# Kernel optimization log

Hardware: AMD Instinct MI355X
Metric: run time of the kernel (lower is better)

The kernel has to match this reference:

```python
import jax, jax.numpy as jnp
import numpy as np

BH = 32  # block_h
BW = 32  # block_w
M, K, N = 4096, 4096, 4096  # tokens, in_features, out_features


def setup_inputs() -> dict:
    key = jax.random.key(0)
    k1, k2, k3, k4 = jax.random.split(key, 4)
    data = jax.random.normal(k1, (M, K), dtype=jnp.float32)
    weight = jax.random.normal(k2, (N, K), dtype=jnp.float32) * 0.02
    bias = jax.random.normal(k3, (N,), dtype=jnp.float32) * 0.02
    # elementwise 0/1 mask over the weight matrix
    mask = jax.random.randint(k4, (N, K), 0, 2, dtype=jnp.int32)
    # conv bias of the 1x1-channel block-summing conv; chosen so ~half the
    # 32x32 blocks (sum ~ Binomial(1024, 0.5)) end up inactive
    conv_bias = jnp.full((1,), -512.0, dtype=jnp.float32)
    return {"data": data, "weight": weight, "bias": bias, "mask": mask,
            "conv_bias": conv_bias}


def reference(data, weight, bias, mask, conv_bias):
    n_out, n_in = weight.shape
    nH, nW = n_out // BH, n_in // BW
    # conv2d with all-ones (BH,BW) kernel, stride (BH,BW) == per-block sum + bias
    block_sum = mask.astype(jnp.float32).reshape(nH, BH, nW, BW).sum(axis=(1, 3))
    block_mask = (block_sum + conv_bias[0]) > 0  # [nH, nW] bool
    # dds matmul (trans_b=True): zero inactive weight blocks, out = data @ W^T
    w_blocks = weight.reshape(nH, BH, nW, BW)
    w_masked = (w_blocks * block_mask[:, None, :, None].astype(weight.dtype)
                ).reshape(n_out, n_in)
    out = jnp.einsum('mk,nk->mn', data, w_masked) + bias
    return out
```

## Files before the change

### kernel.cpp

```cpp
#include <hip/hip_runtime.h>
#include <hip/hip_bf16.h>
#include <stdint.h>

#define M_DIM 4096
#define N_DIM 4096
#define K_DIM 4096
#define NH 128
#define NW 128
#define NKT 64

typedef short bf16x8 __attribute__((ext_vector_type(8)));
typedef short bf16x4 __attribute__((ext_vector_type(4)));
typedef float f32x4 __attribute__((ext_vector_type(4)));

#define MFMA(a, b, c) __builtin_amdgcn_mfma_f32_16x16x32_bf16((a), (b), (c), 0, 0, 0)

__device__ __forceinline__ short f2bf(float f) {
  union { float f; unsigned u; } c; c.f = f;
  unsigned u = c.u;
  unsigned r = (u + 0x7fffu + ((u >> 16) & 1u)) >> 16;
  return (short)r;
}

__global__ __launch_bounds__(256) void k_block_mask(const int* __restrict__ mask,
                                                    const float* __restrict__ conv_bias,
                                                    int* __restrict__ bm) {
  const int bw = blockIdx.x, bh = blockIdx.y;
  const int t = threadIdx.x;
  const int row = t >> 3;
  const int c4 = (t & 7) << 2;
  const int4* p = (const int4*)(mask + (size_t)(bh * 32 + row) * K_DIM + bw * 32 + c4);
  int4 v = *p;
  int s = v.x + v.y + v.z + v.w;
#pragma unroll
  for (int off = 32; off > 0; off >>= 1) s += __shfl_down(s, off);
  __shared__ int red[4];
  if ((t & 63) == 0) red[t >> 6] = s;
  __syncthreads();
  if (t == 0) {
    float tot = (float)(red[0] + red[1] + red[2] + red[3]) + conv_bias[0];
    bm[bh * NW + bw] = (tot > 0.0f) ? 1 : 0;
  }
}

__global__ __launch_bounds__(256) void k_cvt_data(const float* __restrict__ in,
                                                  short* __restrict__ ob) {
  size_t i = (size_t)blockIdx.x * 256 + threadIdx.x;
  f32x4 v = ((const f32x4*)in)[i];
  bf16x4 o;
  o[0] = f2bf(v[0]); o[1] = f2bf(v[1]); o[2] = f2bf(v[2]); o[3] = f2bf(v[3]);
  ((bf16x4*)ob)[i] = o;
}

__global__ __launch_bounds__(256) void k_cvt_weight(const float* __restrict__ w,
                                                    const int* __restrict__ bm,
                                                    short* __restrict__ ob) {
  size_t i = (size_t)blockIdx.x * 256 + threadIdx.x;
  int n = (int)(i >> 10);
  int k = ((int)i & 1023) << 2;
  float m = bm[((n >> 5) << 7) + (k >> 5)] ? 1.0f : 0.0f;
  f32x4 v = ((const f32x4*)w)[i];
  bf16x4 o;
  o[0] = f2bf(v[0] * m); o[1] = f2bf(v[1] * m);
  o[2] = f2bf(v[2] * m); o[3] = f2bf(v[3] * m);
  ((bf16x4*)ob)[i] = o;
}

__global__ __launch_bounds__(512, 2) void k_gemm256(const short* __restrict__ Ab,
                                                    const short* __restrict__ Bb,
                                                    const float* __restrict__ bias,
                                                    const int* __restrict__ bm,
                                                    float* __restrict__ out) {
  __shared__ short Asm[2][2][256][32];
  __shared__ short Bsm[2][2][256][32];

  const int tid = threadIdx.x;
  const int wid = tid >> 6, lane = tid & 63;
  const int wr = wid >> 2, wc = wid & 3;
  const int r = lane & 15, g0 = lane >> 4;
  const int gs = g0 ^ ((r >> 1) & 3);

  const int swz = (blockIdx.x & 7) * 32 + (blockIdx.x >> 3);
  const int bx = swz & 15, by = swz >> 4;
  const int rowM = by * 256, colN = bx * 256;

  const int srow = tid >> 2;
  const int sseg = (tid & 3) ^ ((tid >> 3) & 3);
  const int swave = wid * 512;

  const short* gA = Ab + (size_t)(rowM + srow) * K_DIM + sseg * 8;
  const short* gB = Bb + (size_t)(colN + srow) * K_DIM + sseg * 8;
  const size_t HOFF = (size_t)128 * K_DIM;

  const int nb0 = (colN >> 5) + wc * 2;
  unsigned long long w00, w01, w10, w11;
  {
    const int* bp = bm + nb0 * NW;
    int v0 = bp[lane], v1 = bp[64 + lane], v2 = bp[128 + lane], v3 = bp[192 + lane];
    w00 = __ballot(v0 != 0); w01 = __ballot(v1 != 0);
    w10 = __ballot(v2 != 0); w11 = __ballot(v3 != 0);
  }
  __builtin_amdgcn_sched_barrier(0);

#define BT(lo, hi, kc) ((int)((((kc) & 64) ? (hi) : (lo)) >> ((kc) & 63)) & 1)

#define GLL(g, l)                                                            \
  __builtin_amdgcn_global_load_lds((const __attribute__((address_space(1))) void*)(g), \
                                   (__attribute__((address_space(3))) void*)(l), 16, 0, 0)
#define STA(BUF, kt, h, ks) GLL(gA + HOFF * (h) + (size_t)(kt) * 64 + (ks) * 32, \
                                &Asm[BUF][ks][(h) * 128][0] + swave)
#define STB(BUF, kt, h, ks) GLL(gB + HOFF * (h) + (size_t)(kt) * 64 + (ks) * 32, \
                                &Bsm[BUF][ks][(h) * 128][0] + swave)

#define LDA(BUF, ks, m) (*(const bf16x8*)&Asm[BUF][ks][wr * 128 + (m) * 16 + r][gs * 8])
#define LDB(BUF, ks, n) (*(const bf16x8*)&Bsm[BUF][ks][wc * 64 + (n) * 16 + r][gs * 8])

#define MF8(AR, nn, bb)                                                      \
  acc[0][nn] = MFMA(AR[0], bb, acc[0][nn]); acc[1][nn] = MFMA(AR[1], bb, acc[1][nn]); \
  acc[2][nn] = MFMA(AR[2], bb, acc[2][nn]); acc[3][nn] = MFMA(AR[3], bb, acc[3][nn]); \
  acc[4][nn] = MFMA(AR[4], bb, acc[4][nn]); acc[5][nn] = MFMA(AR[5], bb, acc[5][nn]); \
  acc[6][nn] = MFMA(AR[6], bb, acc[6][nn]); acc[7][nn] = MFMA(AR[7], bb, acc[7][nn]);

#define BAR __builtin_amdgcn_s_barrier()
#define SB0 __builtin_amdgcn_sched_barrier(0)
#define PRIO1 __builtin_amdgcn_s_setprio(1)
#define PRIO0 __builtin_amdgcn_s_setprio(0)
#define VMW_(N) asm volatile("s_waitcnt vmcnt(" #N ")" ::: "memory")
#define VMW(N) VMW_(N)

#define TILE(BUF, NB, u, SB, SA, SR, VM0, VM2, E0, E1, E2, E3)               \
  {                                                                          \
                            \
    BAR; SB0;                                                                \
    bB[0] = LDB(BUF, 0, 2); bB[1] = LDB(BUF, 0, 3);                          \
    aY[0] = LDA(BUF, 1, 0); aY[1] = LDA(BUF, 1, 1);                          \
    aY[2] = LDA(BUF, 1, 2); aY[3] = LDA(BUF, 1, 3);                          \
    if (E0) { PRIO1; MF8(aX, 0, bA[0]); MF8(aX, 1, bA[1]); PRIO0; }          \
    if (SB) { STB(NB, (u) + 1, 0, 0); STB(NB, (u) + 1, 1, 0); }              \
    VMW(VM0);                                                                \
                            \
    BAR; SB0;                                                                \
    aY[4] = LDA(BUF, 1, 4); aY[5] = LDA(BUF, 1, 5);                          \
    aY[6] = LDA(BUF, 1, 6); aY[7] = LDA(BUF, 1, 7);                          \
    bA[0] = LDB(BUF, 1, 0); bA[1] = LDB(BUF, 1, 1);                          \
    if (E1) { PRIO1; MF8(aX, 2, bB[0]); MF8(aX, 3, bB[1]); PRIO0; }          \
    if (SB) { STB(NB, (u) + 1, 0, 1); STB(NB, (u) + 1, 1, 1); }              \
                          \
    BAR; SB0;                                                                \
    bB[0] = LDB(BUF, 1, 2); bB[1] = LDB(BUF, 1, 3);                          \
    if (E2) { PRIO1; MF8(aY, 0, bA[0]); MF8(aY, 1, bA[1]); PRIO0; }          \
    if (SA) { STA(BUF, (u) + 2, 0, 0); STA(BUF, (u) + 2, 1, 0); }            \
    VMW(VM2);                                                                \
                          \
    BAR; SB0;                                                                \
    if (SR) {                                                                \
      aX[0] = LDA(NB, 0, 0); aX[1] = LDA(NB, 0, 1);                          \
      aX[2] = LDA(NB, 0, 2); aX[3] = LDA(NB, 0, 3);                          \
      aX[4] = LDA(NB, 0, 4); aX[5] = LDA(NB, 0, 5);                          \
      aX[6] = LDA(NB, 0, 6); aX[7] = LDA(NB, 0, 7);                          \
      bA[0] = LDB(NB, 0, 0); bA[1] = LDB(NB, 0, 1);                          \
    }                                                                        \
    if (E3) { PRIO1; MF8(aY, 2, bB[0]); MF8(aY, 3, bB[1]); PRIO0; }          \
    if (SA) { STA(BUF, (u) + 2, 0, 1); STA(BUF, (u) + 2, 1, 1); }            \
  }

  f32x4 acc[8][4];
#pragma unroll
  for (int m = 0; m < 8; ++m)
#pragma unroll
    for (int n = 0; n < 4; ++n) acc[m][n] = (f32x4){0.f, 0.f, 0.f, 0.f};

  bf16x8 aX[8], aY[8], bA[2], bB[2];

  STA(0, 0, 0, 0); STA(0, 0, 1, 0); STA(0, 0, 0, 1); STA(0, 0, 1, 1);
  STB(0, 0, 0, 0); STB(0, 0, 1, 0); STB(0, 0, 0, 1); STB(0, 0, 1, 1);
  STA(1, 1, 0, 0); STA(1, 1, 1, 0); STA(1, 1, 0, 1); STA(1, 1, 1, 1);
  VMW(4);
  BAR; SB0;
  aX[0] = LDA(0, 0, 0); aX[1] = LDA(0, 0, 1); aX[2] = LDA(0, 0, 2);
  aX[3] = LDA(0, 0, 3); aX[4] = LDA(0, 0, 4); aX[5] = LDA(0, 0, 5);
  aX[6] = LDA(0, 0, 6); aX[7] = LDA(0, 0, 7);
  bA[0] = LDB(0, 0, 0); bA[1] = LDB(0, 0, 1);

#pragma unroll 1
  for (int u = 0; u < NKT - 2; u += 2) {
    const int kc = 2 * u;
    TILE(0, 1, u, 1, 1, 1, 6, 4,
         BT(w00, w01, kc),     BT(w10, w11, kc),
         BT(w00, w01, kc + 1), BT(w10, w11, kc + 1));
    TILE(1, 0, u + 1, 1, 1, 1, 6, 4,
         BT(w00, w01, kc + 2), BT(w10, w11, kc + 2),
         BT(w00, w01, kc + 3), BT(w10, w11, kc + 3));
  }
  TILE(0, 1, NKT - 2, 1, 0, 1, 6, 2,
       BT(w00, w01, 124), BT(w10, w11, 124),
       BT(w00, w01, 125), BT(w10, w11, 125));
  TILE(1, 0, NKT - 1, 0, 0, 0, 0, 0,
       BT(w00, w01, 126), BT(w10, w11, 126),
       BT(w00, w01, 127), BT(w10, w11, 127));

  const int orow = rowM + wr * 128;
  const int ocol = colN + wc * 64;
#pragma unroll
  for (int n = 0; n < 4; ++n) {
    int col = ocol + n * 16 + r;
    float bz = bias[col];
#pragma unroll
    for (int m = 0; m < 8; ++m) {
      int row0 = orow + m * 16 + g0 * 4;
#pragma unroll
      for (int j = 0; j < 4; ++j)
        out[(size_t)(row0 + j) * N_DIM + col] = acc[m][n][j] + bz;
    }
  }
#undef TILE
#undef GLL
#undef STA
#undef STB
#undef LDA
#undef LDB
#undef MF8
#undef BAR
#undef SB0
#undef PRIO1
#undef PRIO0
#undef VMW
#undef VMW_
#undef BT
}

__global__ __launch_bounds__(256) void k_naive(const float* __restrict__ A,
                                               const float* __restrict__ W,
                                               const float* __restrict__ bias,
                                               const int* __restrict__ bm,
                                               float* __restrict__ out) {
  int col = blockIdx.x * 16 + (threadIdx.x & 15);
  int row = blockIdx.y * 16 + (threadIdx.x >> 4);
  float s = 0.f;
  for (int kb = 0; kb < K_DIM / 32; ++kb) {
    if (bm[(col >> 5) * NW + kb]) {
      int kbase = kb * 32;
#pragma unroll 8
      for (int k = 0; k < 32; ++k)
        s += A[(size_t)row * K_DIM + kbase + k] * W[(size_t)col * K_DIM + kbase + k];
    }
  }
  out[(size_t)row * N_DIM + col] = s + bias[col];
}

extern "C" void kernel_launch(void* const* d_in, const int* in_sizes, int n_in,
                              void* d_out, int out_size, void* d_ws, size_t ws_size,
                              hipStream_t stream) {
  const float* data = (const float*)d_in[0];
  const float* weight = (const float*)d_in[1];
  const float* bias = (const float*)d_in[2];
  const int* mask = (const int*)d_in[3];
  const float* conv_bias = (const float*)d_in[4];
  float* out = (float*)d_out;

  int* bm = (int*)d_ws;
  const size_t off_a = 65536;
  const size_t off_b = off_a + (size_t)M_DIM * K_DIM * 2;
  const size_t needed = off_b + (size_t)N_DIM * K_DIM * 2;

  k_block_mask<<<dim3(NW, NH), 256, 0, stream>>>(mask, conv_bias, bm);

  if (ws_size >= needed) {
    short* Abf = (short*)((char*)d_ws + off_a);
    short* Wbf = (short*)((char*)d_ws + off_b);
    k_cvt_data<<<dim3((M_DIM * (K_DIM / 4)) / 256), 256, 0, stream>>>(data, Abf);
    k_cvt_weight<<<dim3((N_DIM * (K_DIM / 4)) / 256), 256, 0, stream>>>(weight, bm, Wbf);
    k_gemm256<<<dim3(256), 512, 0, stream>>>(Abf, Wbf, bias, bm, out);
  } else {
    k_naive<<<dim3(N_DIM / 16, M_DIM / 16), 256, 0, stream>>>(data, weight, bias, bm, out);
  }
}
```

Before: 150.0 us.

## Restructure K-loop pipeline to one-tile lookahead with explicit LDS waits

Reworks the per-tile schedule of the main bf16 MFMA loop. Global-to-LDS prefetch now runs only one tile ahead instead of two for A, and each sub-step reads its LDS fragments immediately before a full lgkmcnt(0) wait and barrier. The aY register set and the cross-tile register preload are dropped. This lowers register pressure and simplifies synchronisation, but it removes the overlap between LDS reads and MFMAs and shortens the distance that hides global-load latency, and it adds more barriers per tile.

```diff
diff --git a/kernel.cpp b/kernel.cpp
--- a/kernel.cpp
+++ b/kernel.cpp
@@ -123,45 +123,45 @@
 
 #define BAR __builtin_amdgcn_s_barrier()
 #define SB0 __builtin_amdgcn_sched_barrier(0)
+#define LGKM0 asm volatile("s_waitcnt lgkmcnt(0)" ::: "memory")
 #define PRIO1 __builtin_amdgcn_s_setprio(1)
 #define PRIO0 __builtin_amdgcn_s_setprio(0)
 #define VMW_(N) asm volatile("s_waitcnt vmcnt(" #N ")" ::: "memory")
 #define VMW(N) VMW_(N)
 
-#define TILE(BUF, NB, u, SB, SA, SR, VM0, VM2, E0, E1, E2, E3)               \
+#define TILE(BUF, NB, u, SA, SB, N1, N3, E0, E1, E2, E3)                     \
   {                                                                          \
-                            \
-    BAR; SB0;                                                                \
+    bf16x8 aX[8], bA[2], bB[2];                                              \
+                                                    \
+    aX[0] = LDA(BUF, 0, 0); aX[1] = LDA(BUF, 0, 1); aX[2] = LDA(BUF, 0, 2);  \
+    aX[3] = LDA(BUF, 0, 3); aX[4] = LDA(BUF, 0, 4); aX[5] = LDA(BUF, 0, 5);  \
+    aX[6] = LDA(BUF, 0, 6); aX[7] = LDA(BUF, 0, 7);                          \
+    bA[0] = LDB(BUF, 0, 0); bA[1] = LDB(BUF, 0, 1);                          \
+    if (SA) { STA(NB, (u) + 1, 0, 0); STA(NB, (u) + 1, 1, 0); }              \
+    BAR; LGKM0; SB0;                                                         \
+    if (E0) { PRIO1; MF8(aX, 0, bA[0]); MF8(aX, 1, bA[1]); PRIO0; }          \
+    BAR;                                                                     \
+                                                    \
     bB[0] = LDB(BUF, 0, 2); bB[1] = LDB(BUF, 0, 3);                          \
-    aY[0] = LDA(BUF, 1, 0); aY[1] = LDA(BUF, 1, 1);                          \
-    aY[2] = LDA(BUF, 1, 2); aY[3] = LDA(BUF, 1, 3);                          \
-    if (E0) { PRIO1; MF8(aX, 0, bA[0]); MF8(aX, 1, bA[1]); PRIO0; }          \
+    if (SA) { STA(NB, (u) + 1, 0, 1); STA(NB, (u) + 1, 1, 1); }              \
+    BAR; LGKM0; SB0;                                                         \
+    if (E1) { PRIO1; MF8(aX, 2, bB[0]); MF8(aX, 3, bB[1]); PRIO0; }          \
+    VMW(N1); BAR;                                                            \
+                                                  \
+    aX[0] = LDA(BUF, 1, 0); aX[1] = LDA(BUF, 1, 1); aX[2] = LDA(BUF, 1, 2);  \
+    aX[3] = LDA(BUF, 1, 3); aX[4] = LDA(BUF, 1, 4); aX[5] = LDA(BUF, 1, 5);  \
+    aX[6] = LDA(BUF, 1, 6); aX[7] = LDA(BUF, 1, 7);                          \
+    bA[0] = LDB(BUF, 1, 0); bA[1] = LDB(BUF, 1, 1);                          \
     if (SB) { STB(NB, (u) + 1, 0, 0); STB(NB, (u) + 1, 1, 0); }              \
-    VMW(VM0);                                                                \
-                            \
-    BAR; SB0;                                                                \
-    aY[4] = LDA(BUF, 1, 4); aY[5] = LDA(BUF, 1, 5);                          \
-    aY[6] = LDA(BUF, 1, 6); aY[7] = LDA(BUF, 1, 7);                          \
-    bA[0] = LDB(BUF, 1, 0); bA[1] = LDB(BUF, 1, 1);                          \
-    if (E1) { PRIO1; MF8(aX, 2, bB[0]); MF8(aX, 3, bB[1]); PRIO0; }          \
+    BAR; LGKM0; SB0;                                                         \
+    if (E2) { PRIO1; MF8(aX, 0, bA[0]); MF8(aX, 1, bA[1]); PRIO0; }          \
+    BAR;                                                                     \
+                                                  \
+    bB[0] = LDB(BUF, 1, 2); bB[1] = LDB(BUF, 1, 3);                          \
     if (SB) { STB(NB, (u) + 1, 0, 1); STB(NB, (u) + 1, 1, 1); }              \
-                          \
-    BAR; SB0;                                                                \
-    bB[0] = LDB(BUF, 1, 2); bB[1] = LDB(BUF, 1, 3);                          \
-    if (E2) { PRIO1; MF8(aY, 0, bA[0]); MF8(aY, 1, bA[1]); PRIO0; }          \
-    if (SA) { STA(BUF, (u) + 2, 0, 0); STA(BUF, (u) + 2, 1, 0); }            \
-    VMW(VM2);                                                                \
-                          \
-    BAR; SB0;                                                                \
-    if (SR) {                                                                \
-      aX[0] = LDA(NB, 0, 0); aX[1] = LDA(NB, 0, 1);                          \
-      aX[2] = LDA(NB, 0, 2); aX[3] = LDA(NB, 0, 3);                          \
-      aX[4] = LDA(NB, 0, 4); aX[5] = LDA(NB, 0, 5);                          \
-      aX[6] = LDA(NB, 0, 6); aX[7] = LDA(NB, 0, 7);                          \
-      bA[0] = LDB(NB, 0, 0); bA[1] = LDB(NB, 0, 1);                          \
-    }                                                                        \
-    if (E3) { PRIO1; MF8(aY, 2, bB[0]); MF8(aY, 3, bB[1]); PRIO0; }          \
-    if (SA) { STA(BUF, (u) + 2, 0, 1); STA(BUF, (u) + 2, 1, 1); }            \
+    BAR; LGKM0; SB0;                                                         \
+    if (E3) { PRIO1; MF8(aX, 2, bB[0]); MF8(aX, 3, bB[1]); PRIO0; }          \
+    VMW(N3); BAR;                                                            \
   }
 
   f32x4 acc[8][4];
@@ -169,33 +169,26 @@
   for (int m = 0; m < 8; ++m)
 #pragma unroll
     for (int n = 0; n < 4; ++n) acc[m][n] = (f32x4){0.f, 0.f, 0.f, 0.f};
-
-  bf16x8 aX[8], aY[8], bA[2], bB[2];
 
   STA(0, 0, 0, 0); STA(0, 0, 1, 0); STA(0, 0, 0, 1); STA(0, 0, 1, 1);
   STB(0, 0, 0, 0); STB(0, 0, 1, 0); STB(0, 0, 0, 1); STB(0, 0, 1, 1);
-  STA(1, 1, 0, 0); STA(1, 1, 1, 0); STA(1, 1, 0, 1); STA(1, 1, 1, 1);
-  VMW(4);
+  VMW(0);
   BAR; SB0;
-  aX[0] = LDA(0, 0, 0); aX[1] = LDA(0, 0, 1); aX[2] = LDA(0, 0, 2);
-  aX[3] = LDA(0, 0, 3); aX[4] = LDA(0, 0, 4); aX[5] = LDA(0, 0, 5);
-  aX[6] = LDA(0, 0, 6); aX[7] = LDA(0, 0, 7);
-  bA[0] = LDB(0, 0, 0); bA[1] = LDB(0, 0, 1);
 
 #pragma unroll 1
   for (int u = 0; u < NKT - 2; u += 2) {
     const int kc = 2 * u;
-    TILE(0, 1, u, 1, 1, 1, 6, 4,
+    TILE(0, 1, u, 1, 1, 4, 2,
          BT(w00, w01, kc),     BT(w10, w11, kc),
          BT(w00, w01, kc + 1), BT(w10, w11, kc + 1));
-    TILE(1, 0, u + 1, 1, 1, 1, 6, 4,
+    TILE(1, 0, u + 1, 1, 1, 4, 2,
          BT(w00, w01, kc + 2), BT(w10, w11, kc + 2),
          BT(w00, w01, kc + 3), BT(w10, w11, kc + 3));
   }
-  TILE(0, 1, NKT - 2, 1, 0, 1, 6, 2,
+  TILE(0, 1, NKT - 2, 1, 1, 4, 2,
        BT(w00, w01, 124), BT(w10, w11, 124),
        BT(w00, w01, 125), BT(w10, w11, 125));
-  TILE(1, 0, NKT - 1, 0, 0, 0, 0, 0,
+  TILE(1, 0, NKT - 1, 0, 0, 0, 0,
        BT(w00, w01, 126), BT(w10, w11, 126),
        BT(w00, w01, 127), BT(w10, w11, 127));
 
@@ -222,6 +215,7 @@
 #undef MF8
 #undef BAR
 #undef SB0
+#undef LGKM0
 #undef PRIO1
 #undef PRIO0
 #undef VMW
```

After: 170.7 us. 1.14x slower.
